# Kernel optimization log

Hardware: AMD Instinct MI355X
Metric: run time of the kernel (lower is better)

## Reference

```python
import jax, jax.numpy as jnp
import numpy as np

T, D_IN, H, D_OUT = 20, 4, 768, 1
B = 1024


def setup_inputs() -> dict:
    key = jax.random.key(0)
    ks = jax.random.split(key, 8)
    s = 1.0 / np.sqrt(H)
    return {
        "batch_price": jax.random.normal(ks[0], (B, T, D_IN), jnp.float32),
        "batch_event": jax.random.normal(ks[1], (B, T, H), jnp.float32),
        "W_ih": jax.random.uniform(ks[2], (T, 4 * H, D_IN), jnp.float32, -s, s),
        "W_hh": jax.random.uniform(ks[3], (T, 4 * H, H), jnp.float32, -s, s),
        "b_ih": jax.random.uniform(ks[4], (T, 4 * H), jnp.float32, -s, s),
        "b_hh": jax.random.uniform(ks[5], (T, 4 * H), jnp.float32, -s, s),
        "fc_w": jax.random.uniform(ks[6], (D_OUT, H), jnp.float32, -s, s),
        "fc_b": jax.random.uniform(ks[7], (D_OUT,), jnp.float32, -s, s),
    }


def _lstm_cell(x, h_mat, c, wih, whh, bih, bhh):
    # gates: [B, 4H] in PyTorch LSTMCell order (i, f, g, o)
    gates = x @ wih.T + bih + h_mat @ whh.T + bhh
    i, f, g, o = jnp.split(gates, 4, axis=-1)
    c_next = jax.nn.sigmoid(f) * c + jax.nn.sigmoid(i) * jnp.tanh(g)
    h_next = jax.nn.sigmoid(o) * jnp.tanh(c_next)
    return h_next, c_next


def reference(batch_price, batch_event, W_ih, W_hh, b_ih, b_hh, fc_w, fc_b):
    Bb, Tt, _ = batch_price.shape
    Hh = W_hh.shape[-1]
    # step 0: hx = batch_event[:, 0], cell state = zeros
    h, c = _lstm_cell(batch_price[:, 0], batch_event[:, 0],
                      jnp.zeros((Bb, Hh), batch_price.dtype),
                      W_ih[0], W_hh[0], b_ih[0], b_hh[0])

    def step(carry, inp):
        h, c = carry
        x, ev, wih, whh, bih, bhh = inp
        # faithful to source: hx = torch.sum(batch_event_t + h_prev) -> scalar
        hx = jnp.sum(ev + h)
        h_mat = jnp.broadcast_to(hx, (Bb, Hh))
        h2, c2 = _lstm_cell(x, h_mat, c, wih, whh, bih, bhh)
        return (h2, c2), None

    xs = (jnp.swapaxes(batch_price[:, 1:], 0, 1),  # [T-1, B, D_IN]
          jnp.swapaxes(batch_event[:, 1:], 0, 1),  # [T-1, B, H]
          W_ih[1:], W_hh[1:], b_ih[1:], b_hh[1:])
    (h, c), _ = jax.lax.scan(step, (h, c), xs)
    return h @ fc_w.T + fc_b  # [B, 1]
```

## Files before the change

kernel.cpp:

```cpp
#include <hip/hip_runtime.h>
#include <stdint.h>

#define Bsz 1024
#define Tn  20
#define Hn  768
#define G4n 3072

#define WS_SH    0
#define WS_SEV   32
#define WS_PART  64
#define WS_BCAST 576
#define WS_RS    640
#define WS_BS    62080
#define WS_C     123520
#define WS_EVH   909952
#define WS_EVL   1303168
#define WS_WH    1696384
#define WS_WL    2581120
#define WS_SHP   3465856
#define WS_SEVP  3466624

#define NBC_EV   512
#define NBC_W    1152
#define NBC_Z    3
#define NBC_TOT  (NBC_EV + NBC_W + NBC_Z)

#define NB_GEMM   768
#define NB_ROWSUM 1824
#define NB_SEV    608
#define NB_BIAS   60
#define NB_TOTAL  (NB_GEMM + NB_ROWSUM + NB_SEV + NB_BIAS)

typedef float  floatx4 __attribute__((ext_vector_type(4)));
typedef short  bfrag8  __attribute__((ext_vector_type(8)));

__device__ __forceinline__ float wave_reduce(float v){
#pragma unroll
    for (int o = 32; o > 0; o >>= 1) v += __shfl_down(v, o, 64);
    return v;
}
__device__ __forceinline__ float sigf(float x){ return 1.0f/(1.0f+__expf(-x)); }
__device__ __forceinline__ float tanhfast(float x){ return 2.0f/(1.0f+__expf(-2.0f*x)) - 1.0f; }
__device__ __forceinline__ unsigned short f2bf(float f){
    uint32_t u = __float_as_uint(f);
    return (unsigned short)((u + 0x7fffu + ((u>>16)&1u)) >> 16);
}
__device__ __forceinline__ float bf2f(unsigned short h){ return __uint_as_float(((uint32_t)h)<<16); }
__device__ __forceinline__ uint64_t pack_tv(unsigned t, float v){
    return ((uint64_t)t << 32) | (uint64_t)__float_as_uint(v);
}

__global__ __launch_bounds__(256) void k_conv(
    const float* __restrict__ ev, const float* __restrict__ whh,
    float* __restrict__ ws)
{
    int bid = blockIdx.x, tid = threadIdx.x;
    if (bid < NBC_EV + NBC_W) {
        if (tid >= 192) return;
        int r = tid / 96;
        int i = (tid - r*96) * 8;
        const float* src;
        unsigned short *dh, *dl;
        int prow;
        if (bid < NBC_EV) {
            prow = bid*2 + r;
            src = ev + (size_t)prow*(Tn*Hn) + i;
            dh = (unsigned short*)(ws + WS_EVH);
            dl = (unsigned short*)(ws + WS_EVL);
        } else {
            int p = (bid - NBC_EV)*2 + r;
            int gsel = p / Hn;
            int ga = (gsel==0) ? 0 : (gsel==1 ? 2 : 3);
            int j = ga*Hn + (p - gsel*Hn);
            prow = p;
            src = whh + (size_t)j*Hn + i;
            dh = (unsigned short*)(ws + WS_WH);
            dl = (unsigned short*)(ws + WS_WL);
        }
        int rb = prow >> 4, col = prow & 15;
        int kb = i >> 5, q = (i >> 3) & 3;
        size_t base = (((size_t)(rb*24 + kb))*64 + q*16 + col) * 8;

        float4 v0 = *(const float4*)src;
        float4 v1 = *(const float4*)(src+4);
        float f[8] = {v0.x,v0.y,v0.z,v0.w,v1.x,v1.y,v1.z,v1.w};
        bfrag8 hv, lv;
#pragma unroll
        for (int qq = 0; qq < 8; ++qq) {
            unsigned short hb = f2bf(f[qq]);
            hv[qq] = (short)hb;
            lv[qq] = (short)f2bf(f[qq] - bf2f(hb));
        }
        *(bfrag8*)(dh + base) = hv;
        *(bfrag8*)(dl + base) = lv;
    } else {
        int idx = (bid - NBC_EV - NBC_W)*256 + tid;
        if (idx < 640) ws[idx] = 0.0f;
    }
}

__global__ __launch_bounds__(256) void k_pre(
    const float* __restrict__ price, const float* __restrict__ ev,
    const float* __restrict__ wih,   const float* __restrict__ whh,
    const float* __restrict__ bih,   const float* __restrict__ bhh,
    float* __restrict__ ws)
{
    __shared__ float redk[4];
    int blk = blockIdx.x, tid = threadIdx.x;
    int lane = tid & 63, wid = tid >> 6;

    if (blk < NB_GEMM) {
        float* cbuf = ws + WS_C;
        int bt = blk / 48, kt = blk % 48;
        int b0 = bt*64, k0 = kt*16;
        int w = wid, q = lane >> 4, col = lane & 15;

        const unsigned short* evh = (const unsigned short*)(ws + WS_EVH);
        const unsigned short* evl = (const unsigned short*)(ws + WS_EVL);
        const unsigned short* wh  = (const unsigned short*)(ws + WS_WH);
        const unsigned short* wl  = (const unsigned short*)(ws + WS_WL);

        int rb_a = bt*4 + w;
        const unsigned short* pah = evh + (size_t)rb_a*24*512 + (size_t)lane*8;
        const unsigned short* pal = evl + (size_t)rb_a*24*512 + (size_t)lane*8;
        const unsigned short* pb0h = wh + (size_t)(  0 + kt)*24*512 + (size_t)lane*8;
        const unsigned short* pb0l = wl + (size_t)(  0 + kt)*24*512 + (size_t)lane*8;
        const unsigned short* pb1h = wh + (size_t)( 48 + kt)*24*512 + (size_t)lane*8;
        const unsigned short* pb1l = wl + (size_t)( 48 + kt)*24*512 + (size_t)lane*8;
        const unsigned short* pb2h = wh + (size_t)( 96 + kt)*24*512 + (size_t)lane*8;
        const unsigned short* pb2l = wl + (size_t)( 96 + kt)*24*512 + (size_t)lane*8;

        floatx4 acc0 = (floatx4){0.f,0.f,0.f,0.f};
        floatx4 acc1 = (floatx4){0.f,0.f,0.f,0.f};
        floatx4 acc2 = (floatx4){0.f,0.f,0.f,0.f};

#pragma unroll 4
        for (int kb = 0; kb < 24; ++kb) {
            int off = kb*512;
            bfrag8 ah  = *(const bfrag8*)(pah  + off);
            bfrag8 al  = *(const bfrag8*)(pal  + off);
            bfrag8 b0h = *(const bfrag8*)(pb0h + off);
            bfrag8 b0l = *(const bfrag8*)(pb0l + off);
            acc0 = __builtin_amdgcn_mfma_f32_16x16x32_bf16(ah, b0h, acc0, 0,0,0);
            acc0 = __builtin_amdgcn_mfma_f32_16x16x32_bf16(ah, b0l, acc0, 0,0,0);
            acc0 = __builtin_amdgcn_mfma_f32_16x16x32_bf16(al, b0h, acc0, 0,0,0);
            bfrag8 b1h = *(const bfrag8*)(pb1h + off);
            bfrag8 b1l = *(const bfrag8*)(pb1l + off);
            acc1 = __builtin_amdgcn_mfma_f32_16x16x32_bf16(ah, b1h, acc1, 0,0,0);
            acc1 = __builtin_amdgcn_mfma_f32_16x16x32_bf16(ah, b1l, acc1, 0,0,0);
            acc1 = __builtin_amdgcn_mfma_f32_16x16x32_bf16(al, b1h, acc1, 0,0,0);
            bfrag8 b2h = *(const bfrag8*)(pb2h + off);
            bfrag8 b2l = *(const bfrag8*)(pb2l + off);
            acc2 = __builtin_amdgcn_mfma_f32_16x16x32_bf16(ah, b2h, acc2, 0,0,0);
            acc2 = __builtin_amdgcn_mfma_f32_16x16x32_bf16(ah, b2l, acc2, 0,0,0);
            acc2 = __builtin_amdgcn_mfma_f32_16x16x32_bf16(al, b2h, acc2, 0,0,0);
        }

        int j0 = 0*Hn + k0 + col;
        int j1 = 2*Hn + k0 + col;
        int j2 = 3*Hn + k0 + col;
        float4 w0 = *(const float4*)(wih + (size_t)j0*4);
        float4 w1 = *(const float4*)(wih + (size_t)j1*4);
        float4 w2 = *(const float4*)(wih + (size_t)j2*4);
        float bb0 = bih[j0] + bhh[j0];
        float bb1 = bih[j1] + bhh[j1];
        float bb2 = bih[j2] + bhh[j2];

        float hsum = 0.f;
#pragma unroll
        for (int r = 0; r < 4; ++r) {
            int b = b0 + w*16 + q*4 + r;
            float4 xv = *(const float4*)(price + (size_t)b*(Tn*4));
            float gi = acc0[r] + xv.x*w0.x + xv.y*w0.y + xv.z*w0.z + xv.w*w0.w + bb0;
            float gg = acc1[r] + xv.x*w1.x + xv.y*w1.y + xv.z*w1.z + xv.w*w1.w + bb1;
            float go = acc2[r] + xv.x*w2.x + xv.y*w2.y + xv.z*w2.z + xv.w*w2.w + bb2;
            float c0 = sigf(gi) * tanhfast(gg);
            float h0 = sigf(go) * tanhfast(c0);
            cbuf[(size_t)b*Hn + k0 + col] = c0;
            hsum += h0;
        }
        hsum = wave_reduce(hsum);
        if (lane == 0) redk[w] = hsum;
        __syncthreads();
        if (tid == 0)
            ws[WS_SHP + blk] = redk[0]+redk[1]+redk[2]+redk[3];
        return;
    }

    blk -= NB_GEMM;
    if (blk < NB_ROWSUM) {
        int gw = blk*4 + wid;
        int t  = 1 + gw/384;
        int j0 = (gw - (t-1)*384)*8;
        const float* base = whh + ((size_t)t*G4n + j0)*Hn + (size_t)lane*4;
        float s[8];
#pragma unroll
        for (int r = 0; r < 8; ++r) {
            float4 v0 = *(const float4*)(base + (size_t)r*Hn);
            float4 v1 = *(const float4*)(base + (size_t)r*Hn + 256);
            float4 v2 = *(const float4*)(base + (size_t)r*Hn + 512);
            s[r] = (v0.x+v0.y+v0.z+v0.w) + (v1.x+v1.y+v1.z+v1.w) + (v2.x+v2.y+v2.z+v2.w);
        }
        float* rowsum = ws + WS_RS;
#pragma unroll
        for (int r = 0; r < 8; ++r) {
            float rs = wave_reduce(s[r]);
            if (lane == 0) rowsum[(size_t)t*G4n + j0 + r] = rs;
        }
        return;
    }

    blk -= NB_ROWSUM;
    if (blk < NB_SEV) {
        int gw = blk*4 + wid;
        int t   = 1 + gw/128;
        int b0s = (gw - (t-1)*128)*8;
        float s = 0.f;
#pragma unroll
        for (int r = 0; r < 8; ++r) {
            const float* base = ev + ((size_t)(b0s+r)*Tn + t)*Hn + (size_t)lane*4;
            float4 v0 = *(const float4*)(base);
            float4 v1 = *(const float4*)(base + 256);
            float4 v2 = *(const float4*)(base + 512);
            s += (v0.x+v0.y+v0.z+v0.w) + (v1.x+v1.y+v1.z+v1.w) + (v2.x+v2.y+v2.z+v2.w);
        }
        s = wave_reduce(s);
        if (lane == 0) ws[WS_SEVP + gw] = s;
        return;
    }

    blk -= NB_SEV;
    {
        int idx = blk*256 + tid;
        float4 a = *(const float4*)(bih + (size_t)idx*4);
        float4 b = *(const float4*)(bhh + (size_t)idx*4);
        float4 r4; r4.x=a.x+b.x; r4.y=a.y+b.y; r4.z=a.z+b.z; r4.w=a.w+b.w;
        *(float4*)(ws + WS_BS + (size_t)idx*4) = r4;
    }
}

__global__ __launch_bounds__(768) void k_steps(
    const float* __restrict__ price, const float* __restrict__ wih,
    const float* __restrict__ fcw,   const float* __restrict__ fcb,
    float* __restrict__ ws, float* __restrict__ out)
{
    __shared__ float pr[4][80];
    __shared__ float red[12];
    __shared__ float redF[4][12];
    __shared__ float shx;

    uint64_t* part  = (uint64_t*)(ws + WS_PART);
    uint64_t* bcast = (uint64_t*)(ws + WS_BCAST);
    const float* rowsum  = ws + WS_RS;
    const float* biassum = ws + WS_BS;
    float* cbuf = ws + WS_C;

    int blk = blockIdx.x, tid = threadIdx.x;

    if (blk == 256) {
        if (tid >= 64) return;
        int lane = tid;
        const float* shp  = ws + WS_SHP;
        const float* sevp = ws + WS_SEVP;

        float s = 0.f;
#pragma unroll
        for (int i = 0; i < 12; ++i) s += shp[lane + 64*i];
        s = wave_reduce(s);

        {
            float sv = sevp[lane] + sevp[64 + lane];
            sv = wave_reduce(sv);
            if (lane == 0)
                __hip_atomic_store(bcast, pack_tv(1u, sv + s),
                                   __ATOMIC_RELAXED, __HIP_MEMORY_SCOPE_AGENT);
        }

        for (int t = 2; t < Tn; ++t) {
            float sv = sevp[(t-1)*128 + lane] + sevp[(t-1)*128 + 64 + lane];
            sv = wave_reduce(sv);

            unsigned want = (unsigned)(t-1);
            uint64_t u0,u1,u2,u3;
            for (;;) {
                u0 = __hip_atomic_load(&part[lane*4+0], __ATOMIC_RELAXED, __HIP_MEMORY_SCOPE_AGENT);
                u1 = __hip_atomic_load(&part[lane*4+1], __ATOMIC_RELAXED, __HIP_MEMORY_SCOPE_AGENT);
                u2 = __hip_atomic_load(&part[lane*4+2], __ATOMIC_RELAXED, __HIP_MEMORY_SCOPE_AGENT);
                u3 = __hip_atomic_load(&part[lane*4+3], __ATOMIC_RELAXED, __HIP_MEMORY_SCOPE_AGENT);
                if ((unsigned)(u0>>32)==want && (unsigned)(u1>>32)==want &&
                    (unsigned)(u2>>32)==want && (unsigned)(u3>>32)==want) break;
            }
            float p = __uint_as_float((uint32_t)u0) + __uint_as_float((uint32_t)u1)
                    + __uint_as_float((uint32_t)u2) + __uint_as_float((uint32_t)u3);
            p = wave_reduce(p);
            if (lane == 0)
                __hip_atomic_store(bcast, pack_tv((unsigned)t, sv + p),
                                   __ATOMIC_RELAXED, __HIP_MEMORY_SCOPE_AGENT);
        }
        return;
    }

    int lane = tid & 63, wid = tid >> 6;
    int k = tid;

    if (tid < 320) {
        int e = tid / 80, r = tid - e*80;
        pr[e][r] = price[(size_t)(blk + 256*e)*(Tn*4) + r];
    }

    float c[4];
#pragma unroll
    for (int e = 0; e < 4; ++e)
        c[e] = cbuf[(size_t)(blk + 256*e)*Hn + k];

    float fcwk = fcw[k];
    float fcb0 = fcb[0];

    __syncthreads();

    float hsum_prev = 0.f;
    float vout[4] = {0.f,0.f,0.f,0.f};

    for (int t = 1; t < Tn; ++t) {
        if (t >= 2) {
            float v = wave_reduce(hsum_prev);
            if (lane == 0) red[wid] = v;
            __syncthreads();
            if (tid == 0) {
                float tot = 0.f;
#pragma unroll
                for (int i = 0; i < 12; ++i) tot += red[i];
                __hip_atomic_store(&part[blk], pack_tv((unsigned)(t-1), tot),
                                   __ATOMIC_RELAXED, __HIP_MEMORY_SCOPE_AGENT);
            }
        }

        const float* wih_t = wih + (size_t)t*G4n*4;
        float rsv[4], base[4][4];
#pragma unroll
        for (int g = 0; g < 4; ++g) {
            int j = g*Hn + k;
            float4 wv = *(const float4*)(wih_t + (size_t)j*4);
            rsv[g]   = rowsum[t*G4n + j];
            float bs = biassum[t*G4n + j];
#pragma unroll
            for (int e = 0; e < 4; ++e) {
                base[e][g] = pr[e][t*4+0]*wv.x + pr[e][t*4+1]*wv.y
                           + pr[e][t*4+2]*wv.z + pr[e][t*4+3]*wv.w + bs;
            }
        }

        if (tid == 0) {
            uint64_t u;
            do { u = __hip_atomic_load(bcast, __ATOMIC_RELAXED, __HIP_MEMORY_SCOPE_AGENT); }
            while ((unsigned)(u >> 32) != (unsigned)t);
            shx = __uint_as_float((uint32_t)u);
        }
        __syncthreads();
        float hx = shx;

        float hsum = 0.f;
#pragma unroll
        for (int e = 0; e < 4; ++e) {
            float gi = base[e][0] + hx*rsv[0];
            float gf = base[e][1] + hx*rsv[1];
            float gg = base[e][2] + hx*rsv[2];
            float go = base[e][3] + hx*rsv[3];
            float cn = sigf(gf)*c[e] + sigf(gi)*tanhfast(gg);
            c[e] = cn;
            float h = sigf(go)*tanhfast(cn);
            hsum += h;
            if (t == Tn-1) vout[e] = wave_reduce(h * fcwk);
        }
        hsum_prev = hsum;
    }

    if (lane == 0) {
#pragma unroll
        for (int e = 0; e < 4; ++e) redF[e][wid] = vout[e];
    }
    __syncthreads();
    if (tid < 4) {
        float tot = 0.f;
#pragma unroll
        for (int i = 0; i < 12; ++i) tot += redF[tid][i];
        out[blk + 256*tid] = tot + fcb0;
    }
}

extern "C" void kernel_launch(void* const* d_in, const int* in_sizes, int n_in,
                              void* d_out, int out_size, void* d_ws, size_t ws_size,
                              hipStream_t stream)
{
    const float* price = (const float*)d_in[0];
    const float* ev    = (const float*)d_in[1];
    const float* wih   = (const float*)d_in[2];
    const float* whh   = (const float*)d_in[3];
    const float* bih   = (const float*)d_in[4];
    const float* bhh   = (const float*)d_in[5];
    const float* fcw   = (const float*)d_in[6];
    const float* fcb   = (const float*)d_in[7];
    float* out = (float*)d_out;
    float* ws  = (float*)d_ws;

    k_conv <<<NBC_TOT, 256, 0, stream>>>(ev, whh, ws);
    k_pre  <<<NB_TOTAL, 256, 0, stream>>>(price, ev, wih, whh, bih, bhh, ws);
    k_steps<<<257, 768, 0, stream>>>(price, wih, fcw, fcb, ws, out);
}
```

Measured before the change: 424.5 us.

## Fuse precompute and recurrent step kernels into one persistent kernel with token flags

Merges the separate precompute kernel (step-0 GEMM, W_hh row sums, event sums, bias sums) into the recurrent step kernel. Dedicated producer blocks stream row sums and event sums per timestep and publish them through tagged 64-bit tokens, and the worker blocks spin on those tokens. This lets later timesteps' precompute overlap with the sequential recurrence and removes a kernel launch boundary. The bias-sum buffer and shared price staging are dropped in favour of direct loads. It adds fine-grained spin-waiting and needs all 321 blocks to be co-resident to avoid deadlock, and the conversion kernel now zeroes a much larger token region.

```diff
diff --git a/kernel.cpp b/kernel.cpp
--- a/kernel.cpp
+++ b/kernel.cpp
@@ -6,30 +6,25 @@
 #define Hn  768
 #define G4n 3072
 
-#define WS_SH    0
-#define WS_SEV   32
-#define WS_PART  64
-#define WS_BCAST 576
-#define WS_RS    640
-#define WS_BS    62080
-#define WS_C     123520
-#define WS_EVH   909952
-#define WS_EVL   1303168
-#define WS_WH    1696384
-#define WS_WL    2581120
-#define WS_SHP   3465856
-#define WS_SEVP  3466624
+#define WS_PART  0
+#define WS_BCAST 512
+#define WS_STG   1024
+#define WS_SHP   16384
+#define WS_RSU   32768
+#define WS_CB    262144
+#define WS_EVH   2097152
+#define WS_EVL   2490368
+#define WS_WH    2883584
+#define WS_WL    3768320
 
 #define NBC_EV   512
 #define NBC_W    1152
-#define NBC_Z    3
+#define NBC_Z    1672
 #define NBC_TOT  (NBC_EV + NBC_W + NBC_Z)
 
-#define NB_GEMM   768
-#define NB_ROWSUM 1824
-#define NB_SEV    608
-#define NB_BIAS   60
-#define NB_TOTAL  (NB_GEMM + NB_ROWSUM + NB_SEV + NB_BIAS)
+#define NB_WORK  256
+#define NB_STGB  64
+#define HUB_BLK  (NB_WORK + NB_STGB)
 
 typedef float  floatx4 __attribute__((ext_vector_type(4)));
 typedef short  bfrag8  __attribute__((ext_vector_type(8)));
@@ -48,6 +43,17 @@
 __device__ __forceinline__ float bf2f(unsigned short h){ return __uint_as_float(((uint32_t)h)<<16); }
 __device__ __forceinline__ uint64_t pack_tv(unsigned t, float v){
     return ((uint64_t)t << 32) | (uint64_t)__float_as_uint(v);
+}
+__device__ __forceinline__ uint64_t ld_tok(const uint64_t* p){
+    return __hip_atomic_load(p, __ATOMIC_RELAXED, __HIP_MEMORY_SCOPE_AGENT);
+}
+__device__ __forceinline__ void st_tok(uint64_t* p, uint64_t v){
+    __hip_atomic_store(p, v, __ATOMIC_RELAXED, __HIP_MEMORY_SCOPE_AGENT);
+}
+__device__ __forceinline__ float spin_val(const uint64_t* p, unsigned want){
+    uint64_t u = ld_tok(p);
+    while ((unsigned)(u >> 32) != want) u = ld_tok(p);
+    return __uint_as_float((uint32_t)u);
 }
 
 __global__ __launch_bounds__(256) void k_conv(
@@ -94,33 +100,128 @@
         *(bfrag8*)(dh + base) = hv;
         *(bfrag8*)(dl + base) = lv;
     } else {
-        int idx = (bid - NBC_EV - NBC_W)*256 + tid;
-        if (idx < 640) ws[idx] = 0.0f;
-    }
-}
-
-__global__ __launch_bounds__(256) void k_pre(
+        int zb = bid - NBC_EV - NBC_W;
+        size_t base;
+        if      (zb <  22) base = (size_t)zb*1024;
+        else if (zb < 136) base = (size_t)WS_RSU + (size_t)(zb-22)*1024;
+        else               base = (size_t)WS_CB  + (size_t)(zb-136)*1024;
+        float4 z = {0.f,0.f,0.f,0.f};
+        *(float4*)(ws + base + (size_t)tid*4) = z;
+    }
+}
+
+__global__ __launch_bounds__(768, 6) void k_main(
     const float* __restrict__ price, const float* __restrict__ ev,
     const float* __restrict__ wih,   const float* __restrict__ whh,
     const float* __restrict__ bih,   const float* __restrict__ bhh,
-    float* __restrict__ ws)
+    const float* __restrict__ fcw,   const float* __restrict__ fcb,
+    float* __restrict__ ws, float* __restrict__ out)
 {
-    __shared__ float redk[4];
+    __shared__ float red[12];
+    __shared__ float redF[4][12];
+    __shared__ float shx;
+
+    uint64_t* part  = (uint64_t*)(ws + WS_PART);
+    uint64_t* bcast = (uint64_t*)(ws + WS_BCAST);
+    uint64_t* stg   = (uint64_t*)(ws + WS_STG);
+    uint64_t* shp   = (uint64_t*)(ws + WS_SHP);
+    uint64_t* rsu   = (uint64_t*)(ws + WS_RSU);
+    uint64_t* cb    = (uint64_t*)(ws + WS_CB);
+
     int blk = blockIdx.x, tid = threadIdx.x;
     int lane = tid & 63, wid = tid >> 6;
 
-    if (blk < NB_GEMM) {
-        float* cbuf = ws + WS_C;
-        int bt = blk / 48, kt = blk % 48;
-        int b0 = bt*64, k0 = kt*16;
-        int w = wid, q = lane >> 4, col = lane & 15;
+    if (blk == HUB_BLK) {
+        if (tid >= 64) return;
+        uint64_t u0,u1,u2,u3;
+        for (;;) {
+            u0 = ld_tok(&shp[lane*4+0]); u1 = ld_tok(&shp[lane*4+1]);
+            u2 = ld_tok(&shp[lane*4+2]); u3 = ld_tok(&shp[lane*4+3]);
+            if ((unsigned)(u0>>32)==1u && (unsigned)(u1>>32)==1u &&
+                (unsigned)(u2>>32)==1u && (unsigned)(u3>>32)==1u) break;
+        }
+        float sh0 = wave_reduce(__uint_as_float((uint32_t)u0) + __uint_as_float((uint32_t)u1)
+                              + __uint_as_float((uint32_t)u2) + __uint_as_float((uint32_t)u3));
+        for (int t = 1; t < Tn; ++t) {
+            const uint64_t* sg = &stg[(size_t)(t-1)*256];
+            for (;;) {
+                u0 = ld_tok(&sg[lane*4+0]); u1 = ld_tok(&sg[lane*4+1]);
+                u2 = ld_tok(&sg[lane*4+2]); u3 = ld_tok(&sg[lane*4+3]);
+                if ((unsigned)(u0>>32)==(unsigned)t && (unsigned)(u1>>32)==(unsigned)t &&
+                    (unsigned)(u2>>32)==(unsigned)t && (unsigned)(u3>>32)==(unsigned)t) break;
+            }
+            float sev = wave_reduce(__uint_as_float((uint32_t)u0) + __uint_as_float((uint32_t)u1)
+                                  + __uint_as_float((uint32_t)u2) + __uint_as_float((uint32_t)u3));
+            float hsum;
+            if (t == 1) {
+                hsum = sh0;
+            } else {
+                unsigned want = (unsigned)(t-1);
+                for (;;) {
+                    u0 = ld_tok(&part[lane*4+0]); u1 = ld_tok(&part[lane*4+1]);
+                    u2 = ld_tok(&part[lane*4+2]); u3 = ld_tok(&part[lane*4+3]);
+                    if ((unsigned)(u0>>32)==want && (unsigned)(u1>>32)==want &&
+                        (unsigned)(u2>>32)==want && (unsigned)(u3>>32)==want) break;
+                }
+                hsum = wave_reduce(__uint_as_float((uint32_t)u0) + __uint_as_float((uint32_t)u1)
+                                 + __uint_as_float((uint32_t)u2) + __uint_as_float((uint32_t)u3));
+            }
+            if (lane == 0) st_tok(bcast, pack_tv((unsigned)t, sev + hsum));
+        }
+        return;
+    }
+
+    if (blk >= NB_WORK) {
+        if (tid >= 256) return;
+        int sv = (blk - NB_WORK)*4 + wid;
+        for (int t = 1; t < Tn; ++t) {
+            const float* wt = whh + (size_t)t*G4n*Hn;
+            float rs[12];
+#pragma unroll
+            for (int r = 0; r < 12; ++r) {
+                const float* base = wt + (size_t)(sv*12 + r)*Hn + (size_t)lane*4;
+                float4 v0 = *(const float4*)(base);
+                float4 v1 = *(const float4*)(base + 256);
+                float4 v2 = *(const float4*)(base + 512);
+                rs[r] = (v0.x+v0.y+v0.z+v0.w) + (v1.x+v1.y+v1.z+v1.w) + (v2.x+v2.y+v2.z+v2.w);
+            }
+#pragma unroll
+            for (int r = 0; r < 12; ++r) {
+                float v = wave_reduce(rs[r]);
+                if (lane == 0)
+                    st_tok(&rsu[(size_t)(t-1)*G4n + sv*12 + r], pack_tv((unsigned)t, v));
+            }
+            float s = 0.f;
+#pragma unroll
+            for (int r = 0; r < 4; ++r) {
+                const float* base = ev + ((size_t)(sv*4 + r)*Tn + t)*Hn + (size_t)lane*4;
+                float4 v0 = *(const float4*)(base);
+                float4 v1 = *(const float4*)(base + 256);
+                float4 v2 = *(const float4*)(base + 512);
+                s += (v0.x+v0.y+v0.z+v0.w) + (v1.x+v1.y+v1.z+v1.w) + (v2.x+v2.y+v2.z+v2.w);
+            }
+            s = wave_reduce(s);
+            if (lane == 0)
+                st_tok(&stg[(size_t)(t-1)*256 + sv], pack_tv((unsigned)t, s));
+        }
+        return;
+    }
+
+    int k = tid;
+
+    {
+        int g  = wid >> 2, wg = wid & 3;
+        int tau = 3*blk + g;
+        int bt = tau / 48, kt = tau % 48;
+        int b0 = bt*64;
+        int q = lane >> 4, col = lane & 15;
 
         const unsigned short* evh = (const unsigned short*)(ws + WS_EVH);
         const unsigned short* evl = (const unsigned short*)(ws + WS_EVL);
         const unsigned short* wh  = (const unsigned short*)(ws + WS_WH);
         const unsigned short* wl  = (const unsigned short*)(ws + WS_WL);
 
-        int rb_a = bt*4 + w;
+        int rb_a = bt*4 + wg;
         const unsigned short* pah = evh + (size_t)rb_a*24*512 + (size_t)lane*8;
         const unsigned short* pal = evl + (size_t)rb_a*24*512 + (size_t)lane*8;
         const unsigned short* pb0h = wh + (size_t)(  0 + kt)*24*512 + (size_t)lane*8;
@@ -156,6 +257,7 @@
             acc2 = __builtin_amdgcn_mfma_f32_16x16x32_bf16(al, b2h, acc2, 0,0,0);
         }
 
+        int k0 = kt*16;
         int j0 = 0*Hn + k0 + col;
         int j1 = 2*Hn + k0 + col;
         int j2 = 3*Hn + k0 + col;
@@ -169,155 +271,30 @@
         float hsum = 0.f;
 #pragma unroll
         for (int r = 0; r < 4; ++r) {
-            int b = b0 + w*16 + q*4 + r;
+            int b = b0 + wg*16 + q*4 + r;
             float4 xv = *(const float4*)(price + (size_t)b*(Tn*4));
             float gi = acc0[r] + xv.x*w0.x + xv.y*w0.y + xv.z*w0.z + xv.w*w0.w + bb0;
             float gg = acc1[r] + xv.x*w1.x + xv.y*w1.y + xv.z*w1.z + xv.w*w1.w + bb1;
             float go = acc2[r] + xv.x*w2.x + xv.y*w2.y + xv.z*w2.z + xv.w*w2.w + bb2;
             float c0 = sigf(gi) * tanhfast(gg);
             float h0 = sigf(go) * tanhfast(c0);
-            cbuf[(size_t)b*Hn + k0 + col] = c0;
+            st_tok(&cb[(size_t)b*Hn + k0 + col], pack_tv(1u, c0));
             hsum += h0;
         }
         hsum = wave_reduce(hsum);
-        if (lane == 0) redk[w] = hsum;
+        if (lane == 0) red[wid] = hsum;
         __syncthreads();
-        if (tid == 0)
-            ws[WS_SHP + blk] = redk[0]+redk[1]+redk[2]+redk[3];
-        return;
-    }
-
-    blk -= NB_GEMM;
-    if (blk < NB_ROWSUM) {
-        int gw = blk*4 + wid;
-        int t  = 1 + gw/384;
-        int j0 = (gw - (t-1)*384)*8;
-        const float* base = whh + ((size_t)t*G4n + j0)*Hn + (size_t)lane*4;
-        float s[8];
-#pragma unroll
-        for (int r = 0; r < 8; ++r) {
-            float4 v0 = *(const float4*)(base + (size_t)r*Hn);
-            float4 v1 = *(const float4*)(base + (size_t)r*Hn + 256);
-            float4 v2 = *(const float4*)(base + (size_t)r*Hn + 512);
-            s[r] = (v0.x+v0.y+v0.z+v0.w) + (v1.x+v1.y+v1.z+v1.w) + (v2.x+v2.y+v2.z+v2.w);
-        }
-        float* rowsum = ws + WS_RS;
-#pragma unroll
-        for (int r = 0; r < 8; ++r) {
-            float rs = wave_reduce(s[r]);
-            if (lane == 0) rowsum[(size_t)t*G4n + j0 + r] = rs;
-        }
-        return;
-    }
-
-    blk -= NB_ROWSUM;
-    if (blk < NB_SEV) {
-        int gw = blk*4 + wid;
-        int t   = 1 + gw/128;
-        int b0s = (gw - (t-1)*128)*8;
-        float s = 0.f;
-#pragma unroll
-        for (int r = 0; r < 8; ++r) {
-            const float* base = ev + ((size_t)(b0s+r)*Tn + t)*Hn + (size_t)lane*4;
-            float4 v0 = *(const float4*)(base);
-            float4 v1 = *(const float4*)(base + 256);
-            float4 v2 = *(const float4*)(base + 512);
-            s += (v0.x+v0.y+v0.z+v0.w) + (v1.x+v1.y+v1.z+v1.w) + (v2.x+v2.y+v2.z+v2.w);
-        }
-        s = wave_reduce(s);
-        if (lane == 0) ws[WS_SEVP + gw] = s;
-        return;
-    }
-
-    blk -= NB_SEV;
-    {
-        int idx = blk*256 + tid;
-        float4 a = *(const float4*)(bih + (size_t)idx*4);
-        float4 b = *(const float4*)(bhh + (size_t)idx*4);
-        float4 r4; r4.x=a.x+b.x; r4.y=a.y+b.y; r4.z=a.z+b.z; r4.w=a.w+b.w;
-        *(float4*)(ws + WS_BS + (size_t)idx*4) = r4;
-    }
-}
-
-__global__ __launch_bounds__(768) void k_steps(
-    const float* __restrict__ price, const float* __restrict__ wih,
-    const float* __restrict__ fcw,   const float* __restrict__ fcb,
-    float* __restrict__ ws, float* __restrict__ out)
-{
-    __shared__ float pr[4][80];
-    __shared__ float red[12];
-    __shared__ float redF[4][12];
-    __shared__ float shx;
-
-    uint64_t* part  = (uint64_t*)(ws + WS_PART);
-    uint64_t* bcast = (uint64_t*)(ws + WS_BCAST);
-    const float* rowsum  = ws + WS_RS;
-    const float* biassum = ws + WS_BS;
-    float* cbuf = ws + WS_C;
-
-    int blk = blockIdx.x, tid = threadIdx.x;
-
-    if (blk == 256) {
-        if (tid >= 64) return;
-        int lane = tid;
-        const float* shp  = ws + WS_SHP;
-        const float* sevp = ws + WS_SEVP;
-
-        float s = 0.f;
-#pragma unroll
-        for (int i = 0; i < 12; ++i) s += shp[lane + 64*i];
-        s = wave_reduce(s);
-
-        {
-            float sv = sevp[lane] + sevp[64 + lane];
-            sv = wave_reduce(sv);
-            if (lane == 0)
-                __hip_atomic_store(bcast, pack_tv(1u, sv + s),
-                                   __ATOMIC_RELAXED, __HIP_MEMORY_SCOPE_AGENT);
-        }
-
-        for (int t = 2; t < Tn; ++t) {
-            float sv = sevp[(t-1)*128 + lane] + sevp[(t-1)*128 + 64 + lane];
-            sv = wave_reduce(sv);
-
-            unsigned want = (unsigned)(t-1);
-            uint64_t u0,u1,u2,u3;
-            for (;;) {
-                u0 = __hip_atomic_load(&part[lane*4+0], __ATOMIC_RELAXED, __HIP_MEMORY_SCOPE_AGENT);
-                u1 = __hip_atomic_load(&part[lane*4+1], __ATOMIC_RELAXED, __HIP_MEMORY_SCOPE_AGENT);
-                u2 = __hip_atomic_load(&part[lane*4+2], __ATOMIC_RELAXED, __HIP_MEMORY_SCOPE_AGENT);
-                u3 = __hip_atomic_load(&part[lane*4+3], __ATOMIC_RELAXED, __HIP_MEMORY_SCOPE_AGENT);
-                if ((unsigned)(u0>>32)==want && (unsigned)(u1>>32)==want &&
-                    (unsigned)(u2>>32)==want && (unsigned)(u3>>32)==want) break;
-            }
-            float p = __uint_as_float((uint32_t)u0) + __uint_as_float((uint32_t)u1)
-                    + __uint_as_float((uint32_t)u2) + __uint_as_float((uint32_t)u3);
-            p = wave_reduce(p);
-            if (lane == 0)
-                __hip_atomic_store(bcast, pack_tv((unsigned)t, sv + p),
-                                   __ATOMIC_RELAXED, __HIP_MEMORY_SCOPE_AGENT);
-        }
-        return;
-    }
-
-    int lane = tid & 63, wid = tid >> 6;
-    int k = tid;
-
-    if (tid < 320) {
-        int e = tid / 80, r = tid - e*80;
-        pr[e][r] = price[(size_t)(blk + 256*e)*(Tn*4) + r];
+        if (tid == 0) {
+            float tot = 0.f;
+#pragma unroll
+            for (int i = 0; i < 12; ++i) tot += red[i];
+            st_tok(&shp[blk], pack_tv(1u, tot));
+        }
     }
 
     float c[4];
-#pragma unroll
-    for (int e = 0; e < 4; ++e)
-        c[e] = cbuf[(size_t)(blk + 256*e)*Hn + k];
-
     float fcwk = fcw[k];
     float fcb0 = fcb[0];
-
-    __syncthreads();
-
     float hsum_prev = 0.f;
     float vout[4] = {0.f,0.f,0.f,0.f};
 
@@ -330,30 +307,40 @@
                 float tot = 0.f;
 #pragma unroll
                 for (int i = 0; i < 12; ++i) tot += red[i];
-                __hip_atomic_store(&part[blk], pack_tv((unsigned)(t-1), tot),
-                                   __ATOMIC_RELAXED, __HIP_MEMORY_SCOPE_AGENT);
+                st_tok(&part[blk], pack_tv((unsigned)(t-1), tot));
             }
         }
 
         const float* wih_t = wih + (size_t)t*G4n*4;
+        float4 pvv[4];
+#pragma unroll
+        for (int e = 0; e < 4; ++e)
+            pvv[e] = *(const float4*)(price + (size_t)(blk + 256*e)*(Tn*4) + t*4);
+
         float rsv[4], base[4][4];
 #pragma unroll
         for (int g = 0; g < 4; ++g) {
             int j = g*Hn + k;
             float4 wv = *(const float4*)(wih_t + (size_t)j*4);
-            rsv[g]   = rowsum[t*G4n + j];
-            float bs = biassum[t*G4n + j];
+            rsv[g] = spin_val(&rsu[(size_t)(t-1)*G4n + j], (unsigned)t);
+            float bs = bih[(size_t)t*G4n + j] + bhh[(size_t)t*G4n + j];
 #pragma unroll
             for (int e = 0; e < 4; ++e) {
-                base[e][g] = pr[e][t*4+0]*wv.x + pr[e][t*4+1]*wv.y
-                           + pr[e][t*4+2]*wv.z + pr[e][t*4+3]*wv.w + bs;
-            }
+                base[e][g] = pvv[e].x*wv.x + pvv[e].y*wv.y
+                           + pvv[e].z*wv.z + pvv[e].w*wv.w + bs;
+            }
+        }
+
+        if (t == 1) {
+#pragma unroll
+            for (int e = 0; e < 4; ++e)
+                c[e] = spin_val(&cb[(size_t)(blk + 256*e)*Hn + k], 1u);
         }
 
         if (tid == 0) {
             uint64_t u;
-            do { u = __hip_atomic_load(bcast, __ATOMIC_RELAXED, __HIP_MEMORY_SCOPE_AGENT); }
-            while ((unsigned)(u >> 32) != (unsigned)t);
+            do { u = ld_tok(bcast); }
+            while ((unsigned)(u >> 32) < (unsigned)t);
             shx = __uint_as_float((uint32_t)u);
         }
         __syncthreads();
@@ -403,7 +390,7 @@
     float* out = (float*)d_out;
     float* ws  = (float*)d_ws;
 
-    k_conv <<<NBC_TOT, 256, 0, stream>>>(ev, whh, ws);
-    k_pre  <<<NB_TOTAL, 256, 0, stream>>>(price, ev, wih, whh, bih, bhh, ws);
-    k_steps<<<257, 768, 0, stream>>>(price, wih, fcw, fcb, ws, out);
-}
+    k_conv<<<NBC_TOT, 256, 0, stream>>>(ev, whh, ws);
+    k_main<<<HUB_BLK + 1, 768, 0, stream>>>(price, ev, wih, whh, bih, bhh,
+                                            fcw, fcb, ws, out);
+}
```

After: 908.4 us. +114.0%, slower.
